# Performance work log

Hardware: AMD Instinct MI355X
Metric: run time of the kernel (lower is better)

Reference implementation:

```python
import jax, jax.numpy as jnp
import numpy as np

N_NODES = 100000
N_HIDDEN = 128
N_EDGES = 625000
EPS = 1e-12  # F.normalize default eps


def setup_inputs() -> dict:
    key = jax.random.key(0)
    k1, k2, k3 = jax.random.split(key, 3)
    emb = jax.random.normal(k1, (N_NODES, N_HIDDEN), dtype=jnp.float32)
    edge_src = jax.random.randint(k2, (N_EDGES,), 0, N_NODES, dtype=jnp.int64)
    edge_dst = jax.random.randint(k3, (N_EDGES,), 0, N_NODES, dtype=jnp.int64)
    d = jnp.ones((N_HIDDEN,), dtype=jnp.float32)
    scale = jnp.ones((1,), dtype=jnp.float32)
    return {"emb": emb, "edge_src": edge_src, "edge_dst": edge_dst, "d": d, "scale": scale}


def reference(emb, edge_src, edge_dst, d, scale):
    # L2 normalize rows (torch F.normalize: x / max(||x||, eps))
    norm = jnp.linalg.norm(emb, axis=1, keepdims=True)
    e = emb / jnp.maximum(norm, EPS)            # [N, H]
    ew = e * d                                  # diag scale, [N, H]
    # edge-wise u_dot_v: sum over feature dim of ew[src] * e[dst]
    z = jnp.sum(ew[edge_src] * e[edge_dst], axis=1, keepdims=True)  # [E, 1]
    return z * scale
```

## Files before the change

kernel.cpp:

```cpp
#include <hip/hip_runtime.h>

#define NORM_EPS 1e-12f

__device__ __forceinline__ float bf16_lo_to_f(unsigned u) {
    union { unsigned u; float f; } c; c.u = u << 16; return c.f;
}
__device__ __forceinline__ float bf16_hi_to_f(unsigned u) {
    union { unsigned u; float f; } c; c.u = u & 0xFFFF0000u; return c.f;
}
__device__ __forceinline__ unsigned f_to_bf16_rne(float f) {
    union { float f; unsigned u; } c; c.f = f;
    return (c.u + 0x7FFFu + ((c.u >> 16) & 1u)) >> 16;
}

__global__ void norm_bf16_kernel(const float* __restrict__ emb,
                                 unsigned* __restrict__ tbl,
                                 int n_nodes) {
    int wave = (blockIdx.x * blockDim.x + threadIdx.x) >> 6;
    int lane = threadIdx.x & 63;
    if (wave >= n_nodes) return;
    const float2* p = (const float2*)(emb + (size_t)wave * 128);
    float2 v = p[lane];
    float s = v.x * v.x + v.y * v.y;
    #pragma unroll
    for (int off = 32; off > 0; off >>= 1)
        s += __shfl_xor(s, off);
    float inv = 1.0f / fmaxf(sqrtf(s), NORM_EPS);
    unsigned lo = f_to_bf16_rne(v.x * inv);
    unsigned hi = f_to_bf16_rne(v.y * inv);
    tbl[(size_t)wave * 64 + lane] = lo | (hi << 16);
}

__device__ __forceinline__ float dot8(uint4 a, uint4 b, float4 w0, float4 w1) {
    float s;
    s  = bf16_lo_to_f(a.x) * bf16_lo_to_f(b.x) * w0.x;
    s += bf16_hi_to_f(a.x) * bf16_hi_to_f(b.x) * w0.y;
    s += bf16_lo_to_f(a.y) * bf16_lo_to_f(b.y) * w0.z;
    s += bf16_hi_to_f(a.y) * bf16_hi_to_f(b.y) * w0.w;
    s += bf16_lo_to_f(a.z) * bf16_lo_to_f(b.z) * w1.x;
    s += bf16_hi_to_f(a.z) * bf16_hi_to_f(b.z) * w1.y;
    s += bf16_lo_to_f(a.w) * bf16_lo_to_f(b.w) * w1.z;
    s += bf16_hi_to_f(a.w) * bf16_hi_to_f(b.w) * w1.w;
    return s;
}

__global__ void edge_dot_bf16_kernel(const uint4* __restrict__ tbl,
                                     const int* __restrict__ esrc,
                                     const int* __restrict__ edst,
                                     const float* __restrict__ dvec,
                                     const float* __restrict__ scale,
                                     float* __restrict__ out,
                                     int n_edges) {
    int g    = (blockIdx.x * blockDim.x + threadIdx.x) >> 4;
    int lane = threadIdx.x & 15;
    int e0 = g * 2, e1 = e0 + 1;
    if (e0 >= n_edges) return;
    bool has1 = e1 < n_edges;

    int s0 = esrc[e0], t0 = edst[e0];
    int s1 = has1 ? esrc[e1] : s0;
    int t1 = has1 ? edst[e1] : t0;

    uint4 a0 = tbl[(size_t)s0 * 16 + lane];
    uint4 b0 = tbl[(size_t)t0 * 16 + lane];
    uint4 a1 = tbl[(size_t)s1 * 16 + lane];
    uint4 b1 = tbl[(size_t)t1 * 16 + lane];

    const float4* dv = (const float4*)dvec;
    float4 w0 = dv[lane * 2];
    float4 w1 = dv[lane * 2 + 1];

    float acc0 = dot8(a0, b0, w0, w1);
    float acc1 = dot8(a1, b1, w0, w1);

    #pragma unroll
    for (int off = 8; off > 0; off >>= 1) {
        acc0 += __shfl_xor(acc0, off);
        acc1 += __shfl_xor(acc1, off);
    }

    if (lane == 0) {
        float sc = scale[0];
        out[e0] = acc0 * sc;
        if (has1) out[e1] = acc1 * sc;
    }
}

extern "C" void kernel_launch(void* const* d_in, const int* in_sizes, int n_in,
                              void* d_out, int out_size, void* d_ws, size_t ws_size,
                              hipStream_t stream) {
    const float* emb   = (const float*)d_in[0];
    const int*   esrc  = (const int*)d_in[1];
    const int*   edst  = (const int*)d_in[2];
    const float* dvec  = (const float*)d_in[3];
    const float* scale = (const float*)d_in[4];
    float*       out   = (float*)d_out;

    int n_nodes = in_sizes[0] / 128;
    int n_edges = in_sizes[1];

    unsigned* tbl = (unsigned*)d_ws;

    {
        int blocks = (n_nodes + 3) / 4;
        norm_bf16_kernel<<<blocks, 256, 0, stream>>>(emb, tbl, n_nodes);
    }
    {
        int n_pairs = (n_edges + 1) / 2;
        long long threads = (long long)n_pairs * 16;
        int blocks = (int)((threads + 255) / 256);
        edge_dot_bf16_kernel<<<blocks, 256, 0, stream>>>(
            (const uint4*)tbl, esrc, edst, dvec, scale, out, n_edges);
    }
}
```

Baseline: 137.5 us.

## Quantize normalized embeddings to per-row int8 and use sdot4 for edge dots

```diff
diff --git a/kernel.cpp b/kernel.cpp
--- a/kernel.cpp
+++ b/kernel.cpp
@@ -2,57 +2,76 @@
 
 #define NORM_EPS 1e-12f
 
-__device__ __forceinline__ float bf16_lo_to_f(unsigned u) {
-    union { unsigned u; float f; } c; c.u = u << 16; return c.f;
+#if defined(__has_builtin) && __has_builtin(__builtin_amdgcn_sdot4)
+__device__ __forceinline__ int sdot4(unsigned a, unsigned b, int c) {
+    return __builtin_amdgcn_sdot4((int)a, (int)b, c, false);
 }
-__device__ __forceinline__ float bf16_hi_to_f(unsigned u) {
-    union { unsigned u; float f; } c; c.u = u & 0xFFFF0000u; return c.f;
+#else
+__device__ __forceinline__ int sdot4(unsigned a, unsigned b, int c) {
+    #pragma unroll
+    for (int i = 0; i < 4; ++i)
+        c += (int)(signed char)(a >> (8 * i)) * (int)(signed char)(b >> (8 * i));
+    return c;
 }
-__device__ __forceinline__ unsigned f_to_bf16_rne(float f) {
-    union { float f; unsigned u; } c; c.f = f;
-    return (c.u + 0x7FFFu + ((c.u >> 16) & 1u)) >> 16;
-}
+#endif
 
-__global__ void norm_bf16_kernel(const float* __restrict__ emb,
-                                 unsigned* __restrict__ tbl,
-                                 int n_nodes) {
-    int wave = (blockIdx.x * blockDim.x + threadIdx.x) >> 6;
+__global__ void build_tables_kernel(const float* __restrict__ emb,
+                                    const float* __restrict__ dvec,
+                                    unsigned short* __restrict__ tblW,
+                                    unsigned short* __restrict__ tblE,
+                                    float* __restrict__ sclW,
+                                    float* __restrict__ sclE,
+                                    int n_nodes) {
+    int row  = (blockIdx.x * blockDim.x + threadIdx.x) >> 6;
     int lane = threadIdx.x & 63;
-    if (wave >= n_nodes) return;
-    const float2* p = (const float2*)(emb + (size_t)wave * 128);
+    if (row >= n_nodes) return;
+
+    const float2* p = (const float2*)(emb + (size_t)row * 128);
     float2 v = p[lane];
     float s = v.x * v.x + v.y * v.y;
     #pragma unroll
     for (int off = 32; off > 0; off >>= 1)
         s += __shfl_xor(s, off);
     float inv = 1.0f / fmaxf(sqrtf(s), NORM_EPS);
-    unsigned lo = f_to_bf16_rne(v.x * inv);
-    unsigned hi = f_to_bf16_rne(v.y * inv);
-    tbl[(size_t)wave * 64 + lane] = lo | (hi << 16);
+
+    float e0 = v.x * inv, e1 = v.y * inv;
+    float2 d2 = ((const float2*)dvec)[lane];
+    float w0 = e0 * d2.x, w1 = e1 * d2.y;
+
+    float mW = fmaxf(fabsf(w0), fabsf(w1));
+    float mE = fmaxf(fabsf(e0), fabsf(e1));
+    #pragma unroll
+    for (int off = 32; off > 0; off >>= 1) {
+        mW = fmaxf(mW, __shfl_xor(mW, off));
+        mE = fmaxf(mE, __shfl_xor(mE, off));
+    }
+
+    float qW = (mW > 0.f) ? 127.0f / mW : 0.f;
+    float qE = (mE > 0.f) ? 127.0f / mE : 0.f;
+    int qw0 = __float2int_rn(w0 * qW), qw1 = __float2int_rn(w1 * qW);
+    int qe0 = __float2int_rn(e0 * qE), qe1 = __float2int_rn(e1 * qE);
+
+    tblW[(size_t)row * 64 + lane] =
+        (unsigned short)((qw0 & 0xFF) | ((qw1 & 0xFF) << 8));
+    tblE[(size_t)row * 64 + lane] =
+        (unsigned short)((qe0 & 0xFF) | ((qe1 & 0xFF) << 8));
+    if (lane == 0) {
+        sclW[row] = mW * (1.0f / 127.0f);
+        sclE[row] = mE * (1.0f / 127.0f);
+    }
 }
 
-__device__ __forceinline__ float dot8(uint4 a, uint4 b, float4 w0, float4 w1) {
-    float s;
-    s  = bf16_lo_to_f(a.x) * bf16_lo_to_f(b.x) * w0.x;
-    s += bf16_hi_to_f(a.x) * bf16_hi_to_f(b.x) * w0.y;
-    s += bf16_lo_to_f(a.y) * bf16_lo_to_f(b.y) * w0.z;
-    s += bf16_hi_to_f(a.y) * bf16_hi_to_f(b.y) * w0.w;
-    s += bf16_lo_to_f(a.z) * bf16_lo_to_f(b.z) * w1.x;
-    s += bf16_hi_to_f(a.z) * bf16_hi_to_f(b.z) * w1.y;
-    s += bf16_lo_to_f(a.w) * bf16_lo_to_f(b.w) * w1.z;
-    s += bf16_hi_to_f(a.w) * bf16_hi_to_f(b.w) * w1.w;
-    return s;
-}
-
-__global__ void edge_dot_bf16_kernel(const uint4* __restrict__ tbl,
-                                     const int* __restrict__ esrc,
-                                     const int* __restrict__ edst,
-                                     const float* __restrict__ dvec,
-                                     const float* __restrict__ scale,
-                                     float* __restrict__ out,
-                                     int n_edges) {
-    int g    = (blockIdx.x * blockDim.x + threadIdx.x) >> 4;
-    int lane = threadIdx.x & 15;
+__global__ void edge_dot_i8_kernel(const uint4* __restrict__ tW,
+                                   const uint4* __restrict__ tE,
+                                   const float* __restrict__ sW,
+                                   const float* __restrict__ sE,
+                                   const int* __restrict__ esrc,
+                                   const int* __restrict__ edst,
+                                   const float* __restrict__ scale,
+                                   float* __restrict__ out,
+                                   int n_edges) {
+    int g    = (blockIdx.x * blockDim.x + threadIdx.x) >> 3;
+    int lane = threadIdx.x & 7;
     int e0 = g * 2, e1 = e0 + 1;
     if (e0 >= n_edges) return;
     bool has1 = e1 < n_edges;
@@ -61,28 +80,30 @@
     int s1 = has1 ? esrc[e1] : s0;
     int t1 = has1 ? edst[e1] : t0;
 
-    uint4 a0 = tbl[(size_t)s0 * 16 + lane];
-    uint4 b0 = tbl[(size_t)t0 * 16 + lane];
-    uint4 a1 = tbl[(size_t)s1 * 16 + lane];
-    uint4 b1 = tbl[(size_t)t1 * 16 + lane];
+    uint4 a0 = tW[(size_t)s0 * 8 + lane];
+    uint4 b0 = tE[(size_t)t0 * 8 + lane];
+    uint4 a1 = tW[(size_t)s1 * 8 + lane];
+    uint4 b1 = tE[(size_t)t1 * 8 + lane];
 
-    const float4* dv = (const float4*)dvec;
-    float4 w0 = dv[lane * 2];
-    float4 w1 = dv[lane * 2 + 1];
+    float ss0 = sW[s0] * sE[t0];
+    float ss1 = sW[s1] * sE[t1];
 
-    float acc0 = dot8(a0, b0, w0, w1);
-    float acc1 = dot8(a1, b1, w0, w1);
+    int i0 = 0, i1 = 0;
+    i0 = sdot4(a0.x, b0.x, i0); i0 = sdot4(a0.y, b0.y, i0);
+    i0 = sdot4(a0.z, b0.z, i0); i0 = sdot4(a0.w, b0.w, i0);
+    i1 = sdot4(a1.x, b1.x, i1); i1 = sdot4(a1.y, b1.y, i1);
+    i1 = sdot4(a1.z, b1.z, i1); i1 = sdot4(a1.w, b1.w, i1);
 
     #pragma unroll
-    for (int off = 8; off > 0; off >>= 1) {
-        acc0 += __shfl_xor(acc0, off);
-        acc1 += __shfl_xor(acc1, off);
+    for (int off = 4; off > 0; off >>= 1) {
+        i0 += __shfl_xor(i0, off);
+        i1 += __shfl_xor(i1, off);
     }
 
     if (lane == 0) {
         float sc = scale[0];
-        out[e0] = acc0 * sc;
-        if (has1) out[e1] = acc1 * sc;
+        out[e0] = (float)i0 * ss0 * sc;
+        if (has1) out[e1] = (float)i1 * ss1 * sc;
     }
 }
 
@@ -99,17 +120,24 @@
     int n_nodes = in_sizes[0] / 128;
     int n_edges = in_sizes[1];
 
-    unsigned* tbl = (unsigned*)d_ws;
+    char* base = (char*)d_ws;
+    size_t tbl_bytes = (size_t)n_nodes * 128;
+    unsigned short* tblW = (unsigned short*)base;
+    unsigned short* tblE = (unsigned short*)(base + tbl_bytes);
+    float*          sclW = (float*)(base + 2 * tbl_bytes);
+    float*          sclE = (float*)(base + 2 * tbl_bytes + (size_t)n_nodes * 4);
 
     {
         int blocks = (n_nodes + 3) / 4;
-        norm_bf16_kernel<<<blocks, 256, 0, stream>>>(emb, tbl, n_nodes);
+        build_tables_kernel<<<blocks, 256, 0, stream>>>(
+            emb, dvec, tblW, tblE, sclW, sclE, n_nodes);
     }
     {
-        int n_pairs = (n_edges + 1) / 2;
-        long long threads = (long long)n_pairs * 16;
+        int n_groups = (n_edges + 1) / 2;
+        long long threads = (long long)n_groups * 8;
         int blocks = (int)((threads + 255) / 256);
-        edge_dot_bf16_kernel<<<blocks, 256, 0, stream>>>(
-            (const uint4*)tbl, esrc, edst, dvec, scale, out, n_edges);
+        edge_dot_i8_kernel<<<blocks, 256, 0, stream>>>(
+            (const uint4*)tblW, (const uint4*)tblE, sclW, sclE,
+            esrc, edst, scale, out, n_edges);
     }
 }
```

Measured after the change: 131.5 us. 4.4% less time.
